# Optimization experiments

Measured on AMD Instinct MI355X. Metric: run time of the kernel, lower is better.

The kernel has to match this reference:

```python
import jax, jax.numpy as jnp
import numpy as np

N_NODES = 50000
N_EDGES = 800000
C = 128
D_IN = 32
T0, T1 = 25000, 25000
OUT = 16


def setup_inputs() -> dict:
    key = jax.random.key(0)
    ks = jax.random.split(key, 16)
    s_in = 1.0 / np.sqrt(D_IN)
    s_c = 1.0 / np.sqrt(C)
    return {
        "feats0": jax.random.normal(ks[0], (T0, D_IN), jnp.float32),
        "feats1": jax.random.normal(ks[1], (T1, D_IN), jnp.float32),
        "enc_w0": jax.random.normal(ks[2], (D_IN, C), jnp.float32) * s_in,
        "enc_b0": jnp.zeros((C,), jnp.float32),
        "enc_w1": jax.random.normal(ks[3], (D_IN, C), jnp.float32) * s_in,
        "enc_b1": jnp.zeros((C,), jnp.float32),
        "w_self0": jax.random.normal(ks[4], (C, C), jnp.float32) * s_c,
        "w_neigh0": jax.random.normal(ks[5], (C, C), jnp.float32) * s_c,
        "b0": jnp.zeros((C,), jnp.float32),
        "w_self1": jax.random.normal(ks[6], (C, C), jnp.float32) * s_c,
        "w_neigh1": jax.random.normal(ks[7], (C, C), jnp.float32) * s_c,
        "b1": jnp.zeros((C,), jnp.float32),
        "head_w": jax.random.normal(ks[8], (C, OUT), jnp.float32) * s_c,
        "head_b": jnp.zeros((OUT,), jnp.float32),
        "node_row_idx": jax.random.randint(ks[9], (N_NODES,), 0, T0 + T1, jnp.int32),
        "edge_index": jax.random.randint(ks[10], (2, N_EDGES), 0, N_NODES, jnp.int32),
    }


def reference(feats0, feats1, enc_w0, enc_b0, enc_w1, enc_b1,
              w_self0, w_neigh0, b0, w_self1, w_neigh1, b1,
              head_w, head_b, node_row_idx, edge_index):
    # Heterogeneous per-table encoding -> [T0+T1, C]
    x0 = feats0 @ enc_w0 + enc_b0
    x1 = feats1 @ enc_w1 + enc_b1
    x_all = jnp.concatenate([x0, x1], axis=0)
    # Irregular gather: each graph node pulls its table row (vectorized form
    # of the Python loop over index_dict/inverse_index_dict in the original)
    x = x_all[node_row_idx]  # [N, C]

    src, dst = edge_index[0], edge_index[1]
    deg = jnp.maximum(
        jax.ops.segment_sum(jnp.ones((N_EDGES,), x.dtype), dst, num_segments=N_NODES),
        1.0)[:, None]

    # GraphSAGE (mean aggr), 2 layers, ReLU between layers
    for ws, wn, bb, act in ((w_self0, w_neigh0, b0, True),
                            (w_self1, w_neigh1, b1, False)):
        agg = jax.ops.segment_sum(x[src], dst, num_segments=N_NODES) / deg
        x = x @ ws + agg @ wn + bb
        if act:
            x = jax.nn.relu(x)

    return x @ head_w + head_b  # [N, OUT]
```

## Files before the change

### kernel.cpp

```cpp
#include <hip/hip_runtime.h>
#include <hip/hip_bf16.h>

#define N_NODES 50000
#define N_EDGES 800000
#define C 128
#define D_IN 32
#define T0 25000
#define OUT_DIM 16
#define NBUCKETS ((N_NODES + 255) / 256)
#define NB1 512
#define CHUNK1 ((N_EDGES + NB1 - 1) / NB1)
#define ENC_BLOCKS 512
#define HIST_BLOCKS 256


typedef __attribute__((ext_vector_type(8))) short short8;
typedef __attribute__((ext_vector_type(4))) float f32x4;

__device__ __forceinline__ unsigned short f2bf(float f) {
    union { float f; unsigned int i; } u; u.f = f;
    unsigned int x = u.i;
    unsigned int r = x + 0x7fffu + ((x >> 16) & 1u);
    return (unsigned short)(r >> 16);
}
__device__ __forceinline__ float bf2f(unsigned short h) {
    union { unsigned int i; float f; } u; u.i = ((unsigned int)h) << 16;
    return u.f;
}
__device__ __forceinline__ float lo_f(unsigned int w) {
    union { unsigned int i; float f; } u; u.i = w << 16;
    return u.f;
}
__device__ __forceinline__ float hi_f(unsigned int w) {
    union { unsigned int i; float f; } u; u.i = w & 0xffff0000u;
    return u.f;
}
__device__ __forceinline__ void async16(void* lds, const void* g) {
    __builtin_amdgcn_global_load_lds(
        (const __attribute__((address_space(1))) void*)g,
        (__attribute__((address_space(3))) void*)lds, 16, 0, 0);
}
__device__ __forceinline__ void add8(float* a, uint4 v) {
    a[0] += lo_f(v.x); a[1] += hi_f(v.x);
    a[2] += lo_f(v.y); a[3] += hi_f(v.y);
    a[4] += lo_f(v.z); a[5] += hi_f(v.z);
    a[6] += lo_f(v.w); a[7] += hi_f(v.w);
}

__global__ __launch_bounds__(256) void encode_hist_kernel(
    const float* __restrict__ feats0, const float* __restrict__ feats1,
    const float* __restrict__ w0, const float* __restrict__ b0,
    const float* __restrict__ w1, const float* __restrict__ b1,
    const int* __restrict__ row_idx,
    unsigned short* __restrict__ xh, unsigned short* __restrict__ xl,
    const int* __restrict__ dst, int* __restrict__ bucket_counts)
{
    if (blockIdx.x >= ENC_BLOCKS) {
        __shared__ int h[NBUCKETS];
        for (int i = threadIdx.x; i < NBUCKETS; i += 256) h[i] = 0;
        __syncthreads();
        int bid = blockIdx.x - ENC_BLOCKS;
        for (int e = bid * 256 + threadIdx.x; e < N_EDGES;
             e += HIST_BLOCKS * 256)
            atomicAdd(&h[dst[e] >> 8], 1);
        __syncthreads();
        for (int i = threadIdx.x; i < NBUCKETS; i += 256)
            if (h[i]) atomicAdd(&bucket_counts[i], h[i]);
        return;
    }

    __shared__ float sw0[D_IN * C];
    __shared__ float sw1[D_IN * C];
    __shared__ float sb0[C];
    __shared__ float sb1[C];
    for (int i = threadIdx.x; i < D_IN * C; i += blockDim.x) {
        sw0[i] = w0[i];
        sw1[i] = w1[i];
    }
    if (threadIdx.x < C) {
        sb0[threadIdx.x] = b0[threadIdx.x];
        sb1[threadIdx.x] = b1[threadIdx.x];
    }
    __syncthreads();

    int j = threadIdx.x & 15;
    int ln = threadIdx.x >> 4;
    for (int n = blockIdx.x * 16 + ln; n < N_NODES; n += ENC_BLOCKS * 16) {
        int r = row_idx[n];
        const float* f = (r < T0) ? (feats0 + (size_t)r * D_IN)
                                  : (feats1 + (size_t)(r - T0) * D_IN);
        const float* W = (r < T0) ? sw0 : sw1;
        const float* B = (r < T0) ? sb0 : sb1;
        float4 f4[8];
#pragma unroll
        for (int i = 0; i < 8; ++i) f4[i] = ((const float4*)f)[i];
        float acc[8];
#pragma unroll
        for (int cc = 0; cc < 8; ++cc) acc[cc] = B[8 * j + cc];
#pragma unroll
        for (int k = 0; k < D_IN; ++k) {
            float fk = ((const float*)f4)[k];
            float4 wa = *(const float4*)&W[k * C + 8 * j];
            float4 wb = *(const float4*)&W[k * C + 8 * j + 4];
            acc[0] += fk * wa.x; acc[1] += fk * wa.y;
            acc[2] += fk * wa.z; acc[3] += fk * wa.w;
            acc[4] += fk * wb.x; acc[5] += fk * wb.y;
            acc[6] += fk * wb.z; acc[7] += fk * wb.w;
        }
        short8 h8, l8;
#pragma unroll
        for (int cc = 0; cc < 8; ++cc) {
            unsigned short hi = f2bf(acc[cc]);
            h8[cc] = (short)hi;
            l8[cc] = (short)f2bf(acc[cc] - bf2f(hi));
        }
        *(short8*)(xh + (size_t)n * 128 + 8 * j) = h8;
        *(short8*)(xl + (size_t)n * 128 + 8 * j) = l8;
    }
}

__global__ __launch_bounds__(256) void prep_weights(
    const float* __restrict__ ws0, const float* __restrict__ wn0,
    const float* __restrict__ ws1, const float* __restrict__ wn1,
    const float* __restrict__ hw,
    unsigned short* __restrict__ BT0, unsigned short* __restrict__ BT1,
    unsigned short* __restrict__ hwbh, unsigned short* __restrict__ hwbl)
{
    int idx = blockIdx.x * 256 + threadIdx.x;
    const int per_layer = 128 * 512;
    if (idx < 2 * per_layer) {
        int lyr = idx / per_layer;
        int rem = idx - lyr * per_layer;
        int n = rem >> 9;
        int k = rem & 511;
        int seg = k >> 7;
        int ch = k & 127;
        const float* W = (lyr == 0) ? ((seg == 1) ? wn0 : ws0)
                                    : ((seg == 1) ? wn1 : ws1);
        float v = W[ch * 128 + n];
        unsigned short hi = f2bf(v);
        unsigned short out = (seg == 3) ? f2bf(v - bf2f(hi)) : hi;
        (lyr == 0 ? BT0 : BT1)[(size_t)n * 512 + k] = out;
        return;
    }
    int jdx = idx - 2 * per_layer;
    if (jdx >= 2 * 16 * 128) return;
    int plane = jdx >> 11;
    int rem = jdx & 2047;
    int n = rem >> 7;
    int k = rem & 127;
    float v = hw[k * OUT_DIM + n];
    unsigned short hi = f2bf(v);
    (plane ? hwbl : hwbh)[n * 136 + k] =
        plane ? f2bf(v - bf2f(hi)) : hi;
}

__global__ __launch_bounds__(256) void scanb_kernel(
    const int* __restrict__ bucket_counts, int* __restrict__ bucket_base,
    int* __restrict__ bucket_cursor, int* __restrict__ offsets)
{
    __shared__ int ws[4];
    int t = threadIdx.x;
    int c = (t < NBUCKETS) ? bucket_counts[t] : 0;
    int lane = t & 63, wid = t >> 6;
    int v = c;
#pragma unroll
    for (int off = 1; off < 64; off <<= 1) {
        int s = __shfl_up(v, off, 64);
        if (lane >= off) v += s;
    }
    if (lane == 63) ws[wid] = v;
    __syncthreads();
    if (t == 0) {
        int run = 0;
#pragma unroll
        for (int j = 0; j < 4; ++j) { int s = ws[j]; ws[j] = run; run += s; }
    }
    __syncthreads();
    int excl = ws[wid] + (v - c);
    if (t < NBUCKETS) {
        bucket_base[t] = excl;
        bucket_cursor[t] = excl;
    }
    if (t == 0) {
        bucket_base[NBUCKETS] = N_EDGES;
        offsets[N_NODES] = N_EDGES;
    }
}

__global__ __launch_bounds__(256) void bucket1_kernel(
    const int* __restrict__ src, const int* __restrict__ dst,
    int* __restrict__ bucket_cursor, uint2* __restrict__ pairs)
{
    __shared__ int hist[NBUCKETS];
    __shared__ int base[NBUCKETS];
    __shared__ int cur[NBUCKETS];
    int tid = threadIdx.x;
    for (int i = tid; i < NBUCKETS; i += 256) { hist[i] = 0; cur[i] = 0; }
    __syncthreads();
    int ebeg = blockIdx.x * CHUNK1;
    int eend = ebeg + CHUNK1;
    if (eend > N_EDGES) eend = N_EDGES;
    for (int e = ebeg + tid; e < eend; e += 256)
        atomicAdd(&hist[dst[e] >> 8], 1);
    __syncthreads();
    for (int i = tid; i < NBUCKETS; i += 256)
        if (hist[i] > 0) base[i] = atomicAdd(&bucket_cursor[i], hist[i]);
    __syncthreads();
    for (int e = ebeg + tid; e < eend; e += 256) {
        int d = dst[e];
        int b = d >> 8;
        int pos = base[b] + atomicAdd(&cur[b], 1);
        pairs[pos] = make_uint2((unsigned)src[e], (unsigned)d);
    }
}

__global__ __launch_bounds__(256) void bucket2_kernel(
    const uint2* __restrict__ pairs, const int* __restrict__ bucket_base,
    int* __restrict__ offsets, float* __restrict__ deg,
    int* __restrict__ src_sorted)
{
    __shared__ int cnt[256];
    __shared__ int noff[256];
    __shared__ int cur[256];
    __shared__ int ws[4];
    int b = blockIdx.x;
    int n0 = b << 8;
    int tid = threadIdx.x;
    int bb = bucket_base[b];
    int be = bucket_base[b + 1];
    cnt[tid] = 0;
    cur[tid] = 0;
    __syncthreads();
    for (int e = bb + tid; e < be; e += 256)
        atomicAdd(&cnt[pairs[e].y & 255], 1);
    __syncthreads();
    int c = cnt[tid];
    int lane = tid & 63, wid = tid >> 6;
    int v = c;
#pragma unroll
    for (int off = 1; off < 64; off <<= 1) {
        int s = __shfl_up(v, off, 64);
        if (lane >= off) v += s;
    }
    if (lane == 63) ws[wid] = v;
    __syncthreads();
    if (tid == 0) {
        int run = 0;
#pragma unroll
        for (int j = 0; j < 4; ++j) { int s = ws[j]; ws[j] = run; run += s; }
    }
    __syncthreads();
    int o = bb + ws[wid] + (v - c);
    noff[tid] = o;
    int n = n0 + tid;
    if (n < N_NODES) {
        offsets[n] = o;
        deg[n] = (float)(c > 0 ? c : 1);
    }
    __syncthreads();
    for (int e = bb + tid; e < be; e += 256) {
        uint2 p = pairs[e];
        int local = p.y & 255;
        int pos = noff[local] + atomicAdd(&cur[local], 1);
        src_sorted[pos] = (int)p.x;
    }
}

__global__ __launch_bounds__(256) void aggregate_kernel(
    const unsigned short* __restrict__ xh, const int* __restrict__ offsets,
    const int* __restrict__ src_sorted, const float* __restrict__ deg,
    unsigned short* __restrict__ ah)
{
    int wave = (blockIdx.x * blockDim.x + threadIdx.x) >> 6;
    int lane = threadIdx.x & 63;
    if (wave >= N_NODES) return;
    int h = lane >> 4;
    int u = lane & 15;
    int beg = offsets[wave];
    int end = offsets[wave + 1];
    float acc[8];
#pragma unroll
    for (int j = 0; j < 8; ++j) acc[j] = 0.f;

    int e = beg;
    for (; e + 16 <= end; e += 16) {
        int sA = src_sorted[e + h];
        int sB = src_sorted[e + 4 + h];
        int sC = src_sorted[e + 8 + h];
        int sD = src_sorted[e + 12 + h];
        uint4 vA = *(const uint4*)(xh + (size_t)sA * 128 + u * 8);
        uint4 vB = *(const uint4*)(xh + (size_t)sB * 128 + u * 8);
        uint4 vC = *(const uint4*)(xh + (size_t)sC * 128 + u * 8);
        uint4 vD = *(const uint4*)(xh + (size_t)sD * 128 + u * 8);
        add8(acc, vA); add8(acc, vB); add8(acc, vC); add8(acc, vD);
    }
    for (; e + 4 <= end; e += 4) {
        int s = src_sorted[e + h];
        uint4 v = *(const uint4*)(xh + (size_t)s * 128 + u * 8);
        add8(acc, v);
    }
    int rem = end - e;
    if (h < rem) {
        int s = src_sorted[e + h];
        uint4 v = *(const uint4*)(xh + (size_t)s * 128 + u * 8);
        add8(acc, v);
    }

#pragma unroll
    for (int j = 0; j < 8; ++j) {
        acc[j] += __shfl_xor(acc[j], 16);
        acc[j] += __shfl_xor(acc[j], 32);
    }
    if (lane < 16) {
        float inv = 1.0f / deg[wave];
        short8 hv;
#pragma unroll
        for (int j = 0; j < 8; ++j)
            hv[j] = (short)f2bf(acc[j] * inv);
        *(short8*)(ah + (size_t)wave * 128 + u * 8) = hv;
    }
}

#define BM 128
__global__ __launch_bounds__(512) void gemm_mfma(
    unsigned short* __restrict__ xh, unsigned short* __restrict__ xl,
    const unsigned short* __restrict__ ah,
    const unsigned short* __restrict__ BT, const float* __restrict__ bias,
    int mode,
    const unsigned short* __restrict__ hwbh,
    const unsigned short* __restrict__ hwbl,
    const float* __restrict__ hb, float* __restrict__ out)
{
    __shared__ uint4 smem4[4096];
    char* As = (char*)smem4;
    char* Bs = (char*)smem4 + 32768;
    __shared__ float bias_s[C];
    __shared__ unsigned short hwh_s[16 * 136];
    __shared__ unsigned short hwl_s[16 * 136];
    __shared__ float hb_s[OUT_DIM];

    int tid = threadIdx.x;
    int w = tid >> 6, l = tid & 63;
    int row0 = blockIdx.x * BM;
    if (tid < C) bias_s[tid] = bias[tid];
    if (mode == 2) {
        for (int i = tid; i < 16 * 136; i += 512) {
            hwh_s[i] = hwbh[i];
            hwl_s[i] = hwbl[i];
        }
        if (tid < OUT_DIM) hb_s[tid] = hb[tid];
    }

    f32x4 acc[2][4];
#pragma unroll
    for (int mt = 0; mt < 2; ++mt)
#pragma unroll
        for (int nt = 0; nt < 4; ++nt)
            acc[mt][nt] = (f32x4)(0.f);

    int wm = w & 3;
    int wn = w >> 2;
    int quad = l >> 4;
    int mrow = l & 15;

    const unsigned short* abases[4] = {xh, ah, xl, xh};

    for (int c = 0; c < 4; ++c) {
        const char* abase = (const char*)abases[c];
#pragma unroll
        for (int i = 0; i < 4; ++i) {
            int off = i * 8192 + tid * 16;
            int rl = off >> 8;
            int row = row0 + rl;
            if (row > N_NODES - 1) row = N_NODES - 1;
            int u = ((off >> 4) & 15) ^ (rl & 15);
            async16(As + off, abase + (size_t)row * 256 + u * 16);
        }
#pragma unroll
        for (int i = 0; i < 4; ++i) {
            int off = i * 8192 + tid * 16;
            int n = off >> 8;
            int u = ((off >> 4) & 15) ^ (n & 15);
            async16(Bs + off, (const char*)BT + (size_t)n * 1024 + c * 256 + u * 16);
        }
        __syncthreads();
#pragma unroll
        for (int ks = 0; ks < 4; ++ks) {
            int cu = ks * 4 + quad;
            int swz = (cu ^ mrow) * 16;
            short8 a0 = *(const short8*)(As + (wm * 32 + mrow) * 256 + swz);
            short8 a1 = *(const short8*)(As + (wm * 32 + 16 + mrow) * 256 + swz);
            short8 b[4];
#pragma unroll
            for (int nt = 0; nt < 4; ++nt)
                b[nt] = *(const short8*)(Bs + (wn * 64 + nt * 16 + mrow) * 256 + swz);
#pragma unroll
            for (int nt = 0; nt < 4; ++nt) {
                acc[0][nt] = __builtin_amdgcn_mfma_f32_16x16x32_bf16(a0, b[nt], acc[0][nt], 0, 0, 0);
                acc[1][nt] = __builtin_amdgcn_mfma_f32_16x16x32_bf16(a1, b[nt], acc[1][nt], 0, 0, 0);
            }
        }
        __syncthreads();
    }

    char* th = (char*)smem4;
    char* tl = (char*)smem4 + 32768;
    int relu = (mode == 1);
#pragma unroll
    for (int mt = 0; mt < 2; ++mt)
#pragma unroll
        for (int nt = 0; nt < 4; ++nt) {
            int col = wn * 64 + nt * 16 + mrow;
#pragma unroll
            for (int r = 0; r < 4; ++r) {
                int rl = wm * 32 + mt * 16 + quad * 4 + r;
                float v = acc[mt][nt][r] + bias_s[col];
                if (relu) v = fmaxf(v, 0.f);
                unsigned short hi = f2bf(v);
                int su = (col >> 3) ^ (rl & 15);
                char* p = th + rl * 256 + su * 16 + (col & 7) * 2;
                *(unsigned short*)p = hi;
                *(unsigned short*)(p + 32768) = f2bf(v - bf2f(hi));
            }
        }
    __syncthreads();

    if (mode == 1) {
#pragma unroll
        for (int i = 0; i < 4; ++i) {
            int off = i * 8192 + tid * 16;
            int rl = off >> 8;
            int su = (((off >> 4) & 15) ^ (rl & 15)) * 16;
            int row = row0 + rl;
            if (row < N_NODES) {
                *(uint4*)((char*)xh + (size_t)row * 256 + (off & 255)) =
                    *(const uint4*)(th + rl * 256 + su);
                *(uint4*)((char*)xl + (size_t)row * 256 + (off & 255)) =
                    *(const uint4*)(tl + rl * 256 + su);
            }
        }
    } else {
        f32x4 hacc = (f32x4)(0.f);
        const char* Ap[3] = {th, tl, th};
        const unsigned short* Bp[3] = {hwh_s, hwh_s, hwl_s};
#pragma unroll
        for (int ps = 0; ps < 3; ++ps) {
#pragma unroll
            for (int ks = 0; ks < 4; ++ks) {
                int su = ((ks * 4 + quad) ^ mrow) * 16;
                short8 a = *(const short8*)(Ap[ps] + (w * 16 + mrow) * 256 + su);
                short8 b = *(const short8*)((const char*)Bp[ps] +
                                            mrow * 272 + ks * 64 + quad * 16);
                hacc = __builtin_amdgcn_mfma_f32_16x16x32_bf16(a, b, hacc, 0, 0, 0);
            }
        }
        float bb = hb_s[mrow];
#pragma unroll
        for (int r = 0; r < 4; ++r) {
            int grow = row0 + w * 16 + quad * 4 + r;
            if (grow < N_NODES)
                out[(size_t)grow * OUT_DIM + mrow] = hacc[r] + bb;
        }
    }
}

extern "C" void kernel_launch(void* const* d_in, const int* in_sizes, int n_in,
                              void* d_out, int out_size, void* d_ws, size_t ws_size,
                              hipStream_t stream)
{
    const float* feats0 = (const float*)d_in[0];
    const float* feats1 = (const float*)d_in[1];
    const float* enc_w0 = (const float*)d_in[2];
    const float* enc_b0 = (const float*)d_in[3];
    const float* enc_w1 = (const float*)d_in[4];
    const float* enc_b1 = (const float*)d_in[5];
    const float* w_self0 = (const float*)d_in[6];
    const float* w_neigh0 = (const float*)d_in[7];
    const float* b0 = (const float*)d_in[8];
    const float* w_self1 = (const float*)d_in[9];
    const float* w_neigh1 = (const float*)d_in[10];
    const float* b1 = (const float*)d_in[11];
    const float* head_w = (const float*)d_in[12];
    const float* head_b = (const float*)d_in[13];
    const int* node_row_idx = (const int*)d_in[14];
    const int* edge_index = (const int*)d_in[15];
    const int* e_src = edge_index;
    const int* e_dst = edge_index + N_EDGES;

    char* p = (char*)d_ws;
    unsigned short* xh = (unsigned short*)p;  p += (size_t)N_NODES * C * 2;
    unsigned short* xl = (unsigned short*)p;  p += (size_t)N_NODES * C * 2;
    unsigned short* ah = (unsigned short*)p;  p += (size_t)N_NODES * C * 2;
    unsigned short* BT0 = (unsigned short*)p; p += (size_t)128 * 512 * 2;
    unsigned short* BT1 = (unsigned short*)p; p += (size_t)128 * 512 * 2;
    unsigned short* hwbh = (unsigned short*)p; p += (size_t)16 * 136 * 2;
    unsigned short* hwbl = (unsigned short*)p; p += (size_t)16 * 136 * 2;
    float* deg = (float*)p;        p += (size_t)N_NODES * 4;
    int* offsets = (int*)p;        p += (size_t)(N_NODES + 8) * 4;
    int* bucket_counts = (int*)p;  p += (size_t)(NBUCKETS + 8) * 4;
    int* bucket_base = (int*)p;    p += (size_t)(NBUCKETS + 8) * 4;
    int* bucket_cursor = (int*)p;  p += (size_t)(NBUCKETS + 8) * 4;
    int* src_sorted = (int*)p;     p += (size_t)N_EDGES * 4;
    uint2* pairs = (uint2*)ah;

    hipMemsetAsync(bucket_counts, 0, (size_t)(NBUCKETS + 8) * 4, stream);

    encode_hist_kernel<<<ENC_BLOCKS + HIST_BLOCKS, 256, 0, stream>>>(
        feats0, feats1, enc_w0, enc_b0, enc_w1, enc_b1, node_row_idx,
        xh, xl, e_dst, bucket_counts);
    prep_weights<<<(2 * 128 * 512 + 2 * 16 * 128 + 255) / 256, 256, 0, stream>>>(
        w_self0, w_neigh0, w_self1, w_neigh1, head_w, BT0, BT1, hwbh, hwbl);

    scanb_kernel<<<1, 256, 0, stream>>>(bucket_counts, bucket_base,
                                        bucket_cursor, offsets);
    bucket1_kernel<<<NB1, 256, 0, stream>>>(e_src, e_dst, bucket_cursor, pairs);
    bucket2_kernel<<<NBUCKETS, 256, 0, stream>>>(pairs, bucket_base, offsets,
                                                 deg, src_sorted);

    aggregate_kernel<<<(N_NODES * 64 + 255) / 256, 256, 0, stream>>>(
        xh, offsets, src_sorted, deg, ah);
    gemm_mfma<<<(N_NODES + BM - 1) / BM, 512, 0, stream>>>(
        xh, xl, ah, BT0, b0, 1, hwbh, hwbl, head_b, (float*)d_out);

    aggregate_kernel<<<(N_NODES * 64 + 255) / 256, 256, 0, stream>>>(
        xh, offsets, src_sorted, deg, ah);
    gemm_mfma<<<(N_NODES + BM - 1) / BM, 512, 0, stream>>>(
        xh, xl, ah, BT1, b1, 2, hwbh, hwbl, head_b, (float*)d_out);
}
```

Baseline: 246.5 us.

## Drop low-bf16 activation plane, fuse weight prep into encode kernel, predicate aggregation loop

Activations are now kept only as a single bf16 plane instead of a hi/lo split pair. This removes the xl writes in the encoder and GEMM epilogue, one of the four K-segments in each layer GEMM, and one of the three head MFMA passes. Weight preprocessing now runs as extra blocks of the encode/histogram kernel, which saves a launch. The aggregation loop is restructured into a single predicated 16-edge loop with clamped indices. The cost is lower numerical accuracy in the activations, which could exceed tolerance.

```diff
diff --git a/kernel.cpp b/kernel.cpp
--- a/kernel.cpp
+++ b/kernel.cpp
@@ -12,6 +12,8 @@
 #define CHUNK1 ((N_EDGES + NB1 - 1) / NB1)
 #define ENC_BLOCKS 512
 #define HIST_BLOCKS 256
+#define PREP_ITEMS (2 * 128 * 384 + 2 * 16 * 128)
+#define PREP_BLOCKS ((PREP_ITEMS + 255) / 256)
 
 
 typedef __attribute__((ext_vector_type(8))) short short8;
@@ -47,14 +49,47 @@
     a[6] += lo_f(v.w); a[7] += hi_f(v.w);
 }
 
-__global__ __launch_bounds__(256) void encode_hist_kernel(
+__global__ __launch_bounds__(256) void encode_hist_prep_kernel(
     const float* __restrict__ feats0, const float* __restrict__ feats1,
     const float* __restrict__ w0, const float* __restrict__ b0,
     const float* __restrict__ w1, const float* __restrict__ b1,
-    const int* __restrict__ row_idx,
-    unsigned short* __restrict__ xh, unsigned short* __restrict__ xl,
-    const int* __restrict__ dst, int* __restrict__ bucket_counts)
-{
+    const int* __restrict__ row_idx, unsigned short* __restrict__ xh,
+    const int* __restrict__ dst, int* __restrict__ bucket_counts,
+    const float* __restrict__ ws0, const float* __restrict__ wn0,
+    const float* __restrict__ ws1, const float* __restrict__ wn1,
+    const float* __restrict__ hw,
+    unsigned short* __restrict__ BT0, unsigned short* __restrict__ BT1,
+    unsigned short* __restrict__ hwbh, unsigned short* __restrict__ hwbl)
+{
+    if (blockIdx.x >= ENC_BLOCKS + HIST_BLOCKS) {
+        int idx = (blockIdx.x - ENC_BLOCKS - HIST_BLOCKS) * 256 + threadIdx.x;
+        const int per_layer = 128 * 384;
+        if (idx < 2 * per_layer) {
+            int lyr = idx / per_layer;
+            int rem = idx - lyr * per_layer;
+            int n = rem / 384;
+            int k = rem - n * 384;
+            int seg = k >> 7;
+            int ch = k & 127;
+            const float* W = (lyr == 0) ? ((seg == 1) ? wn0 : ws0)
+                                        : ((seg == 1) ? wn1 : ws1);
+            float v = W[ch * 128 + n];
+            unsigned short hi = f2bf(v);
+            unsigned short out = (seg == 2) ? f2bf(v - bf2f(hi)) : hi;
+            (lyr == 0 ? BT0 : BT1)[(size_t)n * 384 + k] = out;
+            return;
+        }
+        int jdx = idx - 2 * per_layer;
+        if (jdx >= 2 * 16 * 128) return;
+        int plane = jdx >> 11;
+        int rem = jdx & 2047;
+        int n = rem >> 7;
+        int k = rem & 127;
+        float v = hw[k * OUT_DIM + n];
+        unsigned short hi = f2bf(v);
+        (plane ? hwbl : hwbh)[n * 136 + k] = plane ? f2bf(v - bf2f(hi)) : hi;
+        return;
+    }
     if (blockIdx.x >= ENC_BLOCKS) {
         __shared__ int h[NBUCKETS];
         for (int i = threadIdx.x; i < NBUCKETS; i += 256) h[i] = 0;
@@ -107,52 +142,11 @@
             acc[4] += fk * wb.x; acc[5] += fk * wb.y;
             acc[6] += fk * wb.z; acc[7] += fk * wb.w;
         }
-        short8 h8, l8;
-#pragma unroll
-        for (int cc = 0; cc < 8; ++cc) {
-            unsigned short hi = f2bf(acc[cc]);
-            h8[cc] = (short)hi;
-            l8[cc] = (short)f2bf(acc[cc] - bf2f(hi));
-        }
+        short8 h8;
+#pragma unroll
+        for (int cc = 0; cc < 8; ++cc) h8[cc] = (short)f2bf(acc[cc]);
         *(short8*)(xh + (size_t)n * 128 + 8 * j) = h8;
-        *(short8*)(xl + (size_t)n * 128 + 8 * j) = l8;
-    }
-}
-
-__global__ __launch_bounds__(256) void prep_weights(
-    const float* __restrict__ ws0, const float* __restrict__ wn0,
-    const float* __restrict__ ws1, const float* __restrict__ wn1,
-    const float* __restrict__ hw,
-    unsigned short* __restrict__ BT0, unsigned short* __restrict__ BT1,
-    unsigned short* __restrict__ hwbh, unsigned short* __restrict__ hwbl)
-{
-    int idx = blockIdx.x * 256 + threadIdx.x;
-    const int per_layer = 128 * 512;
-    if (idx < 2 * per_layer) {
-        int lyr = idx / per_layer;
-        int rem = idx - lyr * per_layer;
-        int n = rem >> 9;
-        int k = rem & 511;
-        int seg = k >> 7;
-        int ch = k & 127;
-        const float* W = (lyr == 0) ? ((seg == 1) ? wn0 : ws0)
-                                    : ((seg == 1) ? wn1 : ws1);
-        float v = W[ch * 128 + n];
-        unsigned short hi = f2bf(v);
-        unsigned short out = (seg == 3) ? f2bf(v - bf2f(hi)) : hi;
-        (lyr == 0 ? BT0 : BT1)[(size_t)n * 512 + k] = out;
-        return;
-    }
-    int jdx = idx - 2 * per_layer;
-    if (jdx >= 2 * 16 * 128) return;
-    int plane = jdx >> 11;
-    int rem = jdx & 2047;
-    int n = rem >> 7;
-    int k = rem & 127;
-    float v = hw[k * OUT_DIM + n];
-    unsigned short hi = f2bf(v);
-    (plane ? hwbl : hwbh)[n * 136 + k] =
-        plane ? f2bf(v - bf2f(hi)) : hi;
+    }
 }
 
 __global__ __launch_bounds__(256) void scanb_kernel(
@@ -283,28 +277,27 @@
 #pragma unroll
     for (int j = 0; j < 8; ++j) acc[j] = 0.f;
 
-    int e = beg;
-    for (; e + 16 <= end; e += 16) {
-        int sA = src_sorted[e + h];
-        int sB = src_sorted[e + 4 + h];
-        int sC = src_sorted[e + 8 + h];
-        int sD = src_sorted[e + 12 + h];
-        uint4 vA = *(const uint4*)(xh + (size_t)sA * 128 + u * 8);
-        uint4 vB = *(const uint4*)(xh + (size_t)sB * 128 + u * 8);
-        uint4 vC = *(const uint4*)(xh + (size_t)sC * 128 + u * 8);
-        uint4 vD = *(const uint4*)(xh + (size_t)sD * 128 + u * 8);
-        add8(acc, vA); add8(acc, vB); add8(acc, vC); add8(acc, vD);
-    }
-    for (; e + 4 <= end; e += 4) {
-        int s = src_sorted[e + h];
-        uint4 v = *(const uint4*)(xh + (size_t)s * 128 + u * 8);
-        add8(acc, v);
-    }
-    int rem = end - e;
-    if (h < rem) {
-        int s = src_sorted[e + h];
-        uint4 v = *(const uint4*)(xh + (size_t)s * 128 + u * 8);
-        add8(acc, v);
+    for (int e = beg; e < end; e += 16) {
+        int i0 = e + h;
+        int i1 = e + 4 + h;
+        int i2 = e + 8 + h;
+        int i3 = e + 12 + h;
+        int c0 = i0 < end ? i0 : beg;
+        int c1 = i1 < end ? i1 : beg;
+        int c2 = i2 < end ? i2 : beg;
+        int c3 = i3 < end ? i3 : beg;
+        int s0 = src_sorted[c0];
+        int s1 = src_sorted[c1];
+        int s2 = src_sorted[c2];
+        int s3 = src_sorted[c3];
+        uint4 v0 = *(const uint4*)(xh + (size_t)s0 * 128 + u * 8);
+        uint4 v1 = *(const uint4*)(xh + (size_t)s1 * 128 + u * 8);
+        uint4 v2 = *(const uint4*)(xh + (size_t)s2 * 128 + u * 8);
+        uint4 v3 = *(const uint4*)(xh + (size_t)s3 * 128 + u * 8);
+        if (i0 < end) add8(acc, v0);
+        if (i1 < end) add8(acc, v1);
+        if (i2 < end) add8(acc, v2);
+        if (i3 < end) add8(acc, v3);
     }
 
 #pragma unroll
@@ -324,8 +317,7 @@
 
 #define BM 128
 __global__ __launch_bounds__(512) void gemm_mfma(
-    unsigned short* __restrict__ xh, unsigned short* __restrict__ xl,
-    const unsigned short* __restrict__ ah,
+    unsigned short* __restrict__ xh, const unsigned short* __restrict__ ah,
     const unsigned short* __restrict__ BT, const float* __restrict__ bias,
     int mode,
     const unsigned short* __restrict__ hwbh,
@@ -364,9 +356,9 @@
     int quad = l >> 4;
     int mrow = l & 15;
 
-    const unsigned short* abases[4] = {xh, ah, xl, xh};
-
-    for (int c = 0; c < 4; ++c) {
+    const unsigned short* abases[3] = {xh, ah, xh};
+
+    for (int c = 0; c < 3; ++c) {
         const char* abase = (const char*)abases[c];
 #pragma unroll
         for (int i = 0; i < 4; ++i) {
@@ -382,7 +374,7 @@
             int off = i * 8192 + tid * 16;
             int n = off >> 8;
             int u = ((off >> 4) & 15) ^ (n & 15);
-            async16(Bs + off, (const char*)BT + (size_t)n * 1024 + c * 256 + u * 16);
+            async16(Bs + off, (const char*)BT + (size_t)n * 768 + c * 256 + u * 16);
         }
         __syncthreads();
 #pragma unroll
@@ -405,7 +397,6 @@
     }
 
     char* th = (char*)smem4;
-    char* tl = (char*)smem4 + 32768;
     int relu = (mode == 1);
 #pragma unroll
     for (int mt = 0; mt < 2; ++mt)
@@ -417,11 +408,9 @@
                 int rl = wm * 32 + mt * 16 + quad * 4 + r;
                 float v = acc[mt][nt][r] + bias_s[col];
                 if (relu) v = fmaxf(v, 0.f);
-                unsigned short hi = f2bf(v);
                 int su = (col >> 3) ^ (rl & 15);
-                char* p = th + rl * 256 + su * 16 + (col & 7) * 2;
-                *(unsigned short*)p = hi;
-                *(unsigned short*)(p + 32768) = f2bf(v - bf2f(hi));
+                *(unsigned short*)(th + rl * 256 + su * 16 + (col & 7) * 2) =
+                    f2bf(v);
             }
         }
     __syncthreads();
@@ -433,23 +422,19 @@
             int rl = off >> 8;
             int su = (((off >> 4) & 15) ^ (rl & 15)) * 16;
             int row = row0 + rl;
-            if (row < N_NODES) {
+            if (row < N_NODES)
                 *(uint4*)((char*)xh + (size_t)row * 256 + (off & 255)) =
                     *(const uint4*)(th + rl * 256 + su);
-                *(uint4*)((char*)xl + (size_t)row * 256 + (off & 255)) =
-                    *(const uint4*)(tl + rl * 256 + su);
-            }
         }
     } else {
         f32x4 hacc = (f32x4)(0.f);
-        const char* Ap[3] = {th, tl, th};
-        const unsigned short* Bp[3] = {hwh_s, hwh_s, hwl_s};
-#pragma unroll
-        for (int ps = 0; ps < 3; ++ps) {
+        const unsigned short* Bp[2] = {hwh_s, hwl_s};
+#pragma unroll
+        for (int ps = 0; ps < 2; ++ps) {
 #pragma unroll
             for (int ks = 0; ks < 4; ++ks) {
                 int su = ((ks * 4 + quad) ^ mrow) * 16;
-                short8 a = *(const short8*)(Ap[ps] + (w * 16 + mrow) * 256 + su);
+                short8 a = *(const short8*)(th + (w * 16 + mrow) * 256 + su);
                 short8 b = *(const short8*)((const char*)Bp[ps] +
                                             mrow * 272 + ks * 64 + quad * 16);
                 hacc = __builtin_amdgcn_mfma_f32_16x16x32_bf16(a, b, hacc, 0, 0, 0);
@@ -490,10 +475,9 @@
 
     char* p = (char*)d_ws;
     unsigned short* xh = (unsigned short*)p;  p += (size_t)N_NODES * C * 2;
-    unsigned short* xl = (unsigned short*)p;  p += (size_t)N_NODES * C * 2;
     unsigned short* ah = (unsigned short*)p;  p += (size_t)N_NODES * C * 2;
-    unsigned short* BT0 = (unsigned short*)p; p += (size_t)128 * 512 * 2;
-    unsigned short* BT1 = (unsigned short*)p; p += (size_t)128 * 512 * 2;
+    unsigned short* BT0 = (unsigned short*)p; p += (size_t)128 * 384 * 2;
+    unsigned short* BT1 = (unsigned short*)p; p += (size_t)128 * 384 * 2;
     unsigned short* hwbh = (unsigned short*)p; p += (size_t)16 * 136 * 2;
     unsigned short* hwbl = (unsigned short*)p; p += (size_t)16 * 136 * 2;
     float* deg = (float*)p;        p += (size_t)N_NODES * 4;
@@ -506,10 +490,10 @@
 
     hipMemsetAsync(bucket_counts, 0, (size_t)(NBUCKETS + 8) * 4, stream);
 
-    encode_hist_kernel<<<ENC_BLOCKS + HIST_BLOCKS, 256, 0, stream>>>(
-        feats0, feats1, enc_w0, enc_b0, enc_w1, enc_b1, node_row_idx,
-        xh, xl, e_dst, bucket_counts);
-    prep_weights<<<(2 * 128 * 512 + 2 * 16 * 128 + 255) / 256, 256, 0, stream>>>(
+    encode_hist_prep_kernel<<<ENC_BLOCKS + HIST_BLOCKS + PREP_BLOCKS, 256, 0,
+                              stream>>>(
+        feats0, feats1, enc_w0, enc_b0, enc_w1, enc_b1, node_row_idx, xh,
+        e_dst, bucket_counts,
         w_self0, w_neigh0, w_self1, w_neigh1, head_w, BT0, BT1, hwbh, hwbl);
 
     scanb_kernel<<<1, 256, 0, stream>>>(bucket_counts, bucket_base,
@@ -521,10 +505,10 @@
     aggregate_kernel<<<(N_NODES * 64 + 255) / 256, 256, 0, stream>>>(
         xh, offsets, src_sorted, deg, ah);
     gemm_mfma<<<(N_NODES + BM - 1) / BM, 512, 0, stream>>>(
-        xh, xl, ah, BT0, b0, 1, hwbh, hwbl, head_b, (float*)d_out);
+        xh, ah, BT0, b0, 1, hwbh, hwbl, head_b, (float*)d_out);
 
     aggregate_kernel<<<(N_NODES * 64 + 255) / 256, 256, 0, stream>>>(
         xh, offsets, src_sorted, deg, ah);
     gemm_mfma<<<(N_NODES + BM - 1) / BM, 512, 0, stream>>>(
-        xh, xl, ah, BT1, b1, 2, hwbh, hwbl, head_b, (float*)d_out);
-}
+        xh, ah, BT1, b1, 2, hwbh, hwbl, head_b, (float*)d_out);
+}
```

Result: faster. 232.6 us (-5.6%).
